# Optimization experiments

Hardware: AMD Instinct MI355X
Metric: run time of the kernel (lower is better)

The kernel has to match this reference:

```python
import jax, jax.numpy as jnp
import numpy as np
from itertools import combinations, permutations

B = 32768          # batch
LATENT = 9
H = 512            # hidden width
NB_OBJ = 5


def _make_o_ids():
    # 30 predicates: 10 unordered 'close' pairs then 20 ordered 'above' pairs.
    pairs = list(combinations(range(NB_OBJ), 2))
    perms = list(permutations(range(NB_OBJ), 2))
    ids = []
    for k in range(NB_OBJ):
        row = [i for i, p in enumerate(pairs) if k in p]
        row += [10 + i for i, p in enumerate(perms) if k in p]
        ids.append(row)
    return np.asarray(ids, dtype=np.int32)  # [5, 12]

O_IDS = jnp.asarray(_make_o_ids())


def setup_inputs() -> dict:
    key = jax.random.key(0)
    ks = jax.random.split(key, 20)
    w = lambda k, *s: (jax.random.normal(k, s, dtype=jnp.float32) * 0.05)
    return {
        "initial_c": jax.random.uniform(ks[0], (B, 30), dtype=jnp.float32),
        "initial_s": jax.random.normal(ks[1], (B, 15), dtype=jnp.float32),
        "current_c": jax.random.uniform(ks[2], (B, 30), dtype=jnp.float32),
        "eps": jax.random.normal(ks[3], (NB_OBJ, B, LATENT), dtype=jnp.float32),
        # encoder: 44 -> 512 -> 512, heads 512 -> 9
        "enc_W0": w(ks[4], H, 44), "enc_b0": w(ks[5], H),
        "enc_W1": w(ks[6], H, H), "enc_b1": w(ks[7], H),
        "Wm": w(ks[8], LATENT, H), "bm": w(ks[9], LATENT),
        "Wv": w(ks[10], LATENT, H), "bv": w(ks[11], LATENT),
        # decoder: 41 -> 512 -> 512 -> 12 (sigmoid)
        "dec_W0": w(ks[12], H, 41), "dec_b0": w(ks[13], H),
        "dec_W1": w(ks[14], H, H), "dec_b1": w(ks[15], H),
        "dec_W2": w(ks[16], 12, H), "dec_b2": w(ks[17], 12),
    }


def reference(initial_c, initial_s, current_c, eps,
              enc_W0, enc_b0, enc_W1, enc_b1, Wm, bm, Wv, bv,
              dec_W0, dec_b0, dec_W1, dec_b1, dec_W2, dec_b2):
    b = initial_c.shape[0]
    one_hot = jnp.broadcast_to(jnp.eye(NB_OBJ, dtype=initial_c.dtype)[:, None, :],
                               (NB_OBJ, b, NB_OBJ))              # [5,B,5]
    s_rep = jnp.broadcast_to(initial_s[None], (NB_OBJ, b, 15))    # [5,B,15]
    gi = jnp.transpose(initial_c[:, O_IDS], (1, 0, 2))            # [5,B,12]
    gc = jnp.transpose(current_c[:, O_IDS], (1, 0, 2))            # [5,B,12]

    # ---- encoder (ReLU after every layer, incl. last inner) ----
    x = jnp.concatenate([one_hot, s_rep, gi, gc], axis=-1)        # [5,B,44]
    h = jax.nn.relu(jnp.einsum('obi,hi->obh', x, enc_W0) + enc_b0)
    h = jax.nn.relu(jnp.einsum('obi,hi->obh', h, enc_W1) + enc_b1)
    means = jnp.einsum('obi,li->obl', h, Wm) + bm                 # [5,B,9]
    log_var = jnp.einsum('obi,li->obl', h, Wv) + bv               # [5,B,9]

    std = jnp.exp(0.5 * log_var)
    z = eps * std + means                                         # [5,B,9]

    # ---- decoder: ReLU x2, sigmoid head ----
    d = jnp.concatenate([one_hot, z, s_rep, gi], axis=-1)         # [5,B,41]
    h = jax.nn.relu(jnp.einsum('obi,hi->obh', d, dec_W0) + dec_b0)
    h = jax.nn.relu(jnp.einsum('obi,hi->obh', h, dec_W1) + dec_b1)
    recon_x = jax.nn.sigmoid(jnp.einsum('obi,li->obl', h, dec_W2) + dec_b2)  # [5,B,12]

    # scatter-add back into dense [B,30]
    reconstructed = jnp.zeros((b, 30), dtype=recon_x.dtype)
    reconstructed = reconstructed.at[:, O_IDS].add(jnp.transpose(recon_x, (1, 0, 2)))
    return (reconstructed, means, log_var, z)
```

## Files before the change

### kernel.cpp

```cpp
#include <hip/hip_runtime.h>
#include <math.h>

#define BATCH 32768
#define HID   512
#define NOBJ  5
#define TM    64
#define NBT   (BATCH/TM)

typedef __attribute__((ext_vector_type(8))) short bf16x8;
typedef __attribute__((ext_vector_type(4))) float f32x4;

typedef const __attribute__((address_space(1))) void* gas1_t;
typedef __attribute__((address_space(3))) void* las3_t;

__device__ __constant__ int d_OIDS[5][12] = {
  {0,1,2,3, 10,11,12,13,14,18,22,26},
  {0,4,5,6, 10,14,15,16,17,19,23,27},
  {1,4,7,8, 11,15,18,19,20,21,24,28},
  {2,5,7,9, 12,16,20,22,23,24,25,29},
  {3,6,8,9, 13,17,21,25,26,27,28,29}
};

#define UO_EW0   0
#define UO_EW1   (UO_EW0 + 512*64)
#define UO_HEADS (UO_EW1 + 512*512)
#define UO_DW0   (UO_HEADS + 32*512)
#define UO_DW1   (UO_DW0 + 512*64)
#define UO_DW2   (UO_DW1 + 512*512)
#define UO_TOTAL (UO_DW2 + 16*512)

#define OUT_MEANS (BATCH*30)
#define OUT_LV    (OUT_MEANS + NOBJ*BATCH*9)
#define OUT_Z     (OUT_LV    + NOBJ*BATCH*9)

__device__ __forceinline__ unsigned short f2b(float x) {
  unsigned int u = __builtin_bit_cast(unsigned int, x);
  u += 0x7FFFu + ((u >> 16) & 1u);
  return (unsigned short)(u >> 16);
}

__global__ void __launch_bounds__(256)
prep_bf16(const float* __restrict__ eW0, const float* __restrict__ eW1,
          const float* __restrict__ Wm,  const float* __restrict__ Wv,
          const float* __restrict__ dW0, const float* __restrict__ dW1,
          const float* __restrict__ dW2, unsigned short* __restrict__ ws)
{
  for (int i = blockIdx.x*blockDim.x + threadIdx.x; i < UO_TOTAL; i += gridDim.x*blockDim.x) {
    float v = 0.f; int j;
    if (i < UO_EW1) {
      j = i - UO_EW0; int h = j >> 6, k = j & 63;
      if (k < 44) v = eW0[h*44 + k];
    } else if (i < UO_HEADS) {
      j = i - UO_EW1; v = eW1[j];
    } else if (i < UO_DW0) {
      j = i - UO_HEADS; int r = j >> 9, k = j & 511;
      if (r < 9)                  v = Wm[r*512 + k];
      else if (r >= 16 && r < 25) v = Wv[(r-16)*512 + k];
    } else if (i < UO_DW1) {
      j = i - UO_DW0; int h = j >> 6, k = j & 63;
      if (k < 41) v = dW0[h*41 + k];
    } else if (i < UO_DW2) {
      j = i - UO_DW1; v = dW1[j];
    } else {
      j = i - UO_DW2; int r = j >> 9, k = j & 511;
      if (r < 12) v = dW2[r*512 + k];
    }
    ws[i] = f2b(v);
  }
}

template<int KDIM>
__device__ __forceinline__ void stage_B(const unsigned short* __restrict__ Wb, int kt,
                                        unsigned short* buf, int t)
{
  #pragma unroll
  for (int i = 0; i < 4; ++i) {
    const int c   = i*512 + t;
    const int col = c >> 2, j = c & 3;
    const int jp  = j ^ (col & 3);
    const unsigned short* g = Wb + col*KDIM + kt*32 + jp*8;
    unsigned short* l = buf + (i*512 + (t & ~63)) * 8;
    __builtin_amdgcn_global_load_lds((gas1_t)g, (las3_t)l, 16, 0, 0);
  }
}

template<int KT, int ROWW>
__device__ __forceinline__ void layer_mfma(const unsigned short* sIn,
                                           const unsigned short* __restrict__ Wb,
                                           const float* __restrict__ bias,
                                           unsigned short* sOut,
                                           unsigned short* sB,
                                           int wave, int lane, int t)
{
  const int lcol = lane & 15;
  const int kg   = lane >> 4;
  const int lk   = kg * 8;
  const int colbase = wave * 64;

  f32x4 acc[4][4];
  #pragma unroll
  for (int n = 0; n < 4; ++n) {
    const float bv = bias[colbase + n*16 + lcol];
    #pragma unroll
    for (int m = 0; m < 4; ++m) acc[m][n] = (f32x4){bv, bv, bv, bv};
  }

  stage_B<KT*32>(Wb, 0, sB, t);
  __syncthreads();

  int cur = 0;
  #pragma unroll 1
  for (int kt = 0; kt < KT; ++kt) {
    if (kt + 1 < KT) stage_B<KT*32>(Wb, kt + 1, sB + (cur ^ 1)*512*32, t);
    const unsigned short* bb = sB + cur*512*32;
    const int k0 = kt*32 + lk;
    bf16x8 a[4];
    #pragma unroll
    for (int m = 0; m < 4; ++m) {
      const int row = m*16 + lcol;
      a[m] = *(const bf16x8*)&sIn[row*ROWW + (k0 ^ ((row & 7) << 3))];
    }
    #pragma unroll
    for (int n = 0; n < 4; ++n) {
      const int col = colbase + n*16 + lcol;
      const bf16x8 b = *(const bf16x8*)&bb[col*32 + ((kg ^ (col & 3)) * 8)];
      #pragma unroll
      for (int m = 0; m < 4; ++m)
        acc[m][n] = __builtin_amdgcn_mfma_f32_16x16x32_bf16(a[m], b, acc[m][n], 0, 0, 0);
    }
    __syncthreads();
    cur ^= 1;
  }

  const int rbase = kg * 4;
  #pragma unroll
  for (int m = 0; m < 4; ++m)
    #pragma unroll
    for (int n = 0; n < 4; ++n) {
      const int col = colbase + n*16 + lcol;
      #pragma unroll
      for (int r = 0; r < 4; ++r) {
        const int row = m*16 + rbase + r;
        sOut[row*512 + (col ^ ((row & 7) << 3))] = f2b(fmaxf(acc[m][n][r], 0.f));
      }
    }
  __syncthreads();
}

__global__ void __launch_bounds__(512, 2)
vae_mfma(const float* __restrict__ initial_c, const float* __restrict__ initial_s,
         const float* __restrict__ current_c, const float* __restrict__ eps,
         const float* __restrict__ enc_b0, const float* __restrict__ enc_b1,
         const float* __restrict__ bm, const float* __restrict__ bv,
         const float* __restrict__ dec_b0, const float* __restrict__ dec_b1,
         const float* __restrict__ dec_b2, const unsigned short* __restrict__ ws,
         float* __restrict__ out)
{
  __shared__ __align__(16) unsigned short s_act[TM*512];
  __shared__ __align__(16) unsigned short s_bs[2*512*32];
  __shared__ __align__(16) unsigned short s_in[TM*64];

  const int t = threadIdx.x;
  const int wave = t >> 6, lane = t & 63;
  const int lcol = lane & 15, kg = lane >> 4;
  const int lk = kg * 8, rbase = kg * 4;
  const int o     = blockIdx.x / NBT;
  const int bbase = (blockIdx.x % NBT) * TM;

  for (int s = t; s < TM*64; s += 512) {
    const int row = s >> 6, col = s & 63;
    float v = 0.f;
    if (col < 5)       v = (col == o) ? 1.f : 0.f;
    else if (col < 20) v = initial_s[(bbase+row)*15 + col - 5];
    else if (col < 32) v = initial_c[(bbase+row)*30 + d_OIDS[o][col-20]];
    else if (col < 44) v = current_c[(bbase+row)*30 + d_OIDS[o][col-32]];
    s_in[row*64 + (col ^ ((row & 7) << 3))] = f2b(v);
  }
  __syncthreads();

  layer_mfma<2, 64>  (s_in,  ws + UO_EW0, enc_b0, s_act, s_bs, wave, lane, t);
  layer_mfma<16, 512>(s_act, ws + UO_EW1, enc_b1, s_act, s_bs, wave, lane, t);

  {
    for (int s = t; s < TM*64; s += 512) {
      const int row = s >> 6, col = s & 63;
      if (col >= 5 && col < 14) continue;
      float v = 0.f;
      if (col < 5)       v = (col == o) ? 1.f : 0.f;
      else if (col < 29) v = initial_s[(bbase+row)*15 + col - 14];
      else if (col < 41) v = initial_c[(bbase+row)*30 + d_OIDS[o][col-29]];
      s_in[row*64 + (col ^ ((row & 7) << 3))] = f2b(v);
    }
    f32x4 am, av;
    if (wave < 4) {
      const float bmv = (lcol < 9) ? bm[lcol] : 0.f;
      const float bvv = (lcol < 9) ? bv[lcol] : 0.f;
      am = (f32x4){bmv, bmv, bmv, bmv};
      av = (f32x4){bvv, bvv, bvv, bvv};
      const unsigned short* hpM = ws + UO_HEADS + lcol*512 + lk;
      const unsigned short* hpV = hpM + 16*512;
      const int hrow = wave*16 + lcol;
      bf16x8 m0 = *(const bf16x8*)hpM;
      bf16x8 v0 = *(const bf16x8*)hpV;
      #pragma unroll 1
      for (int kt = 0; kt < 16; ++kt) {
        bf16x8 m1 = m0, v1 = v0;
        if (kt + 1 < 16) {
          m1 = *(const bf16x8*)(hpM + (kt+1)*32);
          v1 = *(const bf16x8*)(hpV + (kt+1)*32);
        }
        const int k0 = kt*32 + lk;
        bf16x8 a = *(const bf16x8*)&s_act[hrow*512 + (k0 ^ ((lcol & 7) << 3))];
        am = __builtin_amdgcn_mfma_f32_16x16x32_bf16(a, m0, am, 0, 0, 0);
        av = __builtin_amdgcn_mfma_f32_16x16x32_bf16(a, v0, av, 0, 0, 0);
        m0 = m1; v0 = v1;
      }
    }
    __syncthreads();
    float* stage = (float*)s_bs;
    if (wave < 4 && lcol < 9) {
      #pragma unroll
      for (int r = 0; r < 4; ++r) {
        const int row = wave*16 + rbase + r;
        const int gid = (o*BATCH + bbase + row)*9 + lcol;
        const float m_ = am[r], v_ = av[r];
        const float zz = fmaf(eps[gid], expf(0.5f*v_), m_);
        stage[       row*9 + lcol] = m_;
        stage[576 +  row*9 + lcol] = v_;
        stage[1152 + row*9 + lcol] = zz;
        s_in[row*64 + ((5 + lcol) ^ ((row & 7) << 3))] = f2b(zz);
      }
    }
    __syncthreads();
    const int ob_m = OUT_MEANS + (o*BATCH + bbase)*9;
    const int ob_v = OUT_LV    + (o*BATCH + bbase)*9;
    const int ob_z = OUT_Z     + (o*BATCH + bbase)*9;
    for (int i = t; i < TM*9; i += 512) {
      __builtin_nontemporal_store(stage[i],        &out[ob_m + i]);
      __builtin_nontemporal_store(stage[576 + i],  &out[ob_v + i]);
      __builtin_nontemporal_store(stage[1152 + i], &out[ob_z + i]);
    }
    __syncthreads();
  }

  layer_mfma<2, 64>  (s_in,  ws + UO_DW0, dec_b0, s_act, s_bs, wave, lane, t);
  layer_mfma<16, 512>(s_act, ws + UO_DW1, dec_b1, s_act, s_bs, wave, lane, t);

  if (wave < 4) {
    const float b2 = (lcol < 12) ? dec_b2[lcol] : 0.f;
    f32x4 acc = (f32x4){b2, b2, b2, b2};
    const unsigned short* wp = ws + UO_DW2 + lcol*512 + lk;
    const int hrow = wave*16 + lcol;
    bf16x8 b0 = *(const bf16x8*)wp;
    #pragma unroll 1
    for (int kt = 0; kt < 16; ++kt) {
      bf16x8 b1 = b0;
      if (kt + 1 < 16) b1 = *(const bf16x8*)(wp + (kt+1)*32);
      const int k0 = kt*32 + lk;
      bf16x8 a = *(const bf16x8*)&s_act[hrow*512 + (k0 ^ ((lcol & 7) << 3))];
      acc = __builtin_amdgcn_mfma_f32_16x16x32_bf16(a, b0, acc, 0, 0, 0);
      b0 = b1;
    }
    if (lcol < 12) {
      const int c30 = d_OIDS[o][lcol];
      #pragma unroll
      for (int r = 0; r < 4; ++r) {
        const int row = wave*16 + rbase + r;
        atomicAdd(&out[(bbase + row)*30 + c30], 1.f / (1.f + expf(-acc[r])));
      }
    }
  }
}

__global__ void __launch_bounds__(256)
vae_naive(const float* __restrict__ initial_c, const float* __restrict__ initial_s,
          const float* __restrict__ current_c, const float* __restrict__ eps,
          const float* eW0, const float* eb0, const float* eW1, const float* eb1,
          const float* Wm, const float* bm, const float* Wv, const float* bv,
          const float* dW0, const float* db0, const float* dW1, const float* db1,
          const float* dW2, const float* db2, float* out)
{
  __shared__ float xs[44], ds[41], h1[HID], h2[HID], rec[30];
  const int b = blockIdx.x, t = threadIdx.x;
  if (t < 30) rec[t] = 0.f;
  for (int o = 0; o < NOBJ; ++o) {
    __syncthreads();
    if (t < 44) {
      float v;
      if      (t < 5)  v = (t == o) ? 1.f : 0.f;
      else if (t < 20) v = initial_s[b*15 + (t-5)];
      else if (t < 32) v = initial_c[b*30 + d_OIDS[o][t-20]];
      else             v = current_c[b*30 + d_OIDS[o][t-32]];
      xs[t] = v;
    }
    __syncthreads();
    for (int h = t; h < HID; h += 256) {
      float a = eb0[h];
      for (int k = 0; k < 44; ++k) a = fmaf(xs[k], eW0[h*44+k], a);
      h1[h] = fmaxf(a, 0.f);
    }
    __syncthreads();
    for (int h = t; h < HID; h += 256) {
      float a = eb1[h];
      for (int k = 0; k < HID; ++k) a = fmaf(h1[k], eW1[h*512+k], a);
      h2[h] = fmaxf(a, 0.f);
    }
    __syncthreads();
    if (t < 9) {
      float am = bm[t], av = bv[t];
      for (int k = 0; k < HID; ++k) { am = fmaf(h2[k], Wm[t*512+k], am); av = fmaf(h2[k], Wv[t*512+k], av); }
      const int gid = (o*BATCH + b)*9 + t;
      out[OUT_MEANS + gid] = am;
      out[OUT_LV    + gid] = av;
      const float zz = fmaf(eps[gid], expf(0.5f*av), am);
      out[OUT_Z     + gid] = zz;
      ds[5+t] = zz;
    }
    if (t < 41 && (t < 5 || t >= 14)) {
      float v;
      if      (t < 5)  v = (t == o) ? 1.f : 0.f;
      else if (t < 29) v = initial_s[b*15 + (t-14)];
      else             v = initial_c[b*30 + d_OIDS[o][t-29]];
      ds[t] = v;
    }
    __syncthreads();
    for (int h = t; h < HID; h += 256) {
      float a = db0[h];
      for (int k = 0; k < 41; ++k) a = fmaf(ds[k], dW0[h*41+k], a);
      h1[h] = fmaxf(a, 0.f);
    }
    __syncthreads();
    for (int h = t; h < HID; h += 256) {
      float a = db1[h];
      for (int k = 0; k < HID; ++k) a = fmaf(h1[k], dW1[h*512+k], a);
      h2[h] = fmaxf(a, 0.f);
    }
    __syncthreads();
    if (t < 12) {
      float a = db2[t];
      for (int k = 0; k < HID; ++k) a = fmaf(h2[k], dW2[t*512+k], a);
      rec[d_OIDS[o][t]] += 1.f / (1.f + expf(-a));
    }
  }
  __syncthreads();
  if (t < 30) out[b*30+t] = rec[t];
}

extern "C" void kernel_launch(void* const* d_in, const int* in_sizes, int n_in,
                              void* d_out, int out_size, void* d_ws, size_t ws_size,
                              hipStream_t stream)
{
  const float* initial_c = (const float*)d_in[0];
  const float* initial_s = (const float*)d_in[1];
  const float* current_c = (const float*)d_in[2];
  const float* eps       = (const float*)d_in[3];
  const float* eW0 = (const float*)d_in[4];
  const float* eb0 = (const float*)d_in[5];
  const float* eW1 = (const float*)d_in[6];
  const float* eb1 = (const float*)d_in[7];
  const float* Wm  = (const float*)d_in[8];
  const float* bm  = (const float*)d_in[9];
  const float* Wv  = (const float*)d_in[10];
  const float* bv  = (const float*)d_in[11];
  const float* dW0 = (const float*)d_in[12];
  const float* db0 = (const float*)d_in[13];
  const float* dW1 = (const float*)d_in[14];
  const float* db1 = (const float*)d_in[15];
  const float* dW2 = (const float*)d_in[16];
  const float* db2 = (const float*)d_in[17];
  float* out = (float*)d_out;

  if (ws_size >= (size_t)UO_TOTAL * sizeof(unsigned short)) {
    unsigned short* ws = (unsigned short*)d_ws;
    prep_bf16<<<1024, 256, 0, stream>>>(eW0, eW1, Wm, Wv, dW0, dW1, dW2, ws);
    hipMemsetAsync(out, 0, (size_t)BATCH * 30 * sizeof(float), stream);
    vae_mfma<<<NOBJ*NBT, 512, 0, stream>>>(initial_c, initial_s, current_c, eps,
                                           eb0, eb1, bm, bv, db0, db1, db2, ws, out);
  } else {
    vae_naive<<<BATCH, 256, 0, stream>>>(initial_c, initial_s, current_c, eps,
                                         eW0, eb0, eW1, eb1, Wm, bm, Wv, bv,
                                         dW0, db0, dW1, db1, dW2, db2, out);
  }
}
```

Measured before the change: 447.3 us.

## Triple-buffer weight staging with one barrier per k-step and fragment-ordered LDS layout

Weight tiles now go through a three-slot LDS ring and are prefetched two k-steps ahead. Each step waits on vmcnt with a single barrier instead of two __syncthreads. The staged B layout is rearranged so each lane's fragment is a contiguous 16-byte chunk, which removes the XOR swizzle on reads. MFMA sections run at raised wave priority. s_in is aliased into the third buffer slot to keep LDS usage unchanged, which risks corruption if the input tile is still live while layer 0 stages into that slot. The hand-written vmcnt counts also depend on exactly four outstanding loads per stage.

```diff
diff --git a/kernel.cpp b/kernel.cpp
--- a/kernel.cpp
+++ b/kernel.cpp
@@ -76,10 +76,10 @@
   #pragma unroll
   for (int i = 0; i < 4; ++i) {
     const int c   = i*512 + t;
-    const int col = c >> 2, j = c & 3;
-    const int jp  = j ^ (col & 3);
-    const unsigned short* g = Wb + col*KDIM + kt*32 + jp*8;
-    unsigned short* l = buf + (i*512 + (t & ~63)) * 8;
+    const int col = ((c >> 6) << 4) | (c & 15);
+    const int kg  = (c >> 4) & 3;
+    const unsigned short* g = Wb + col*KDIM + kt*32 + kg*8;
+    unsigned short* l = buf + (size_t)(i*512 + (t & ~63)) * 8;
     __builtin_amdgcn_global_load_lds((gas1_t)g, (las3_t)l, 16, 0, 0);
   }
 }
@@ -96,6 +96,7 @@
   const int kg   = lane >> 4;
   const int lk   = kg * 8;
   const int colbase = wave * 64;
+  const int cb4  = colbase >> 4;
 
   f32x4 acc[4][4];
   #pragma unroll
@@ -105,14 +106,21 @@
     for (int m = 0; m < 4; ++m) acc[m][n] = (f32x4){bv, bv, bv, bv};
   }
 
+  asm volatile("s_waitcnt vmcnt(0)" ::: "memory");
   stage_B<KT*32>(Wb, 0, sB, t);
-  __syncthreads();
+  if (KT > 1) stage_B<KT*32>(Wb, 1, sB + 16384, t);
 
   int cur = 0;
   #pragma unroll 1
   for (int kt = 0; kt < KT; ++kt) {
-    if (kt + 1 < KT) stage_B<KT*32>(Wb, kt + 1, sB + (cur ^ 1)*512*32, t);
-    const unsigned short* bb = sB + cur*512*32;
+    if (kt + 1 < KT) asm volatile("s_waitcnt vmcnt(4)" ::: "memory");
+    else             asm volatile("s_waitcnt vmcnt(0)" ::: "memory");
+    __builtin_amdgcn_s_barrier();
+    __builtin_amdgcn_sched_barrier(0);
+    int s2 = cur + 2; if (s2 >= 3) s2 -= 3;
+    if (kt + 2 < KT) stage_B<KT*32>(Wb, kt + 2, sB + s2*16384, t);
+
+    const unsigned short* bb = sB + cur*16384;
     const int k0 = kt*32 + lk;
     bf16x8 a[4];
     #pragma unroll
@@ -120,18 +128,20 @@
       const int row = m*16 + lcol;
       a[m] = *(const bf16x8*)&sIn[row*ROWW + (k0 ^ ((row & 7) << 3))];
     }
+    __builtin_amdgcn_s_setprio(1);
     #pragma unroll
     for (int n = 0; n < 4; ++n) {
-      const int col = colbase + n*16 + lcol;
-      const bf16x8 b = *(const bf16x8*)&bb[col*32 + ((kg ^ (col & 3)) * 8)];
+      const int chunk = ((cb4 + n)*4 + kg)*16 + lcol;
+      const bf16x8 b = *(const bf16x8*)&bb[chunk*8];
       #pragma unroll
       for (int m = 0; m < 4; ++m)
         acc[m][n] = __builtin_amdgcn_mfma_f32_16x16x32_bf16(a[m], b, acc[m][n], 0, 0, 0);
     }
-    __syncthreads();
-    cur ^= 1;
-  }
-
+    __builtin_amdgcn_s_setprio(0);
+    cur = (cur + 1 == 3) ? 0 : cur + 1;
+  }
+
+  __syncthreads();
   const int rbase = kg * 4;
   #pragma unroll
   for (int m = 0; m < 4; ++m)
@@ -157,8 +167,8 @@
          float* __restrict__ out)
 {
   __shared__ __align__(16) unsigned short s_act[TM*512];
-  __shared__ __align__(16) unsigned short s_bs[2*512*32];
-  __shared__ __align__(16) unsigned short s_in[TM*64];
+  __shared__ __align__(16) unsigned short s_bs[3*16384];
+  unsigned short* s_in = s_bs + 2*16384;
 
   const int t = threadIdx.x;
   const int wave = t >> 6, lane = t & 63;
```

Result: slower. 637.8 us (+42.6%).

## Double the row tile to 128 with a 2x4 wave grid and single-buffered B staging

Applied to the files above, without the earlier changes.

Raises the per-block row tile from 64 to 128 and arranges the 8 waves as a 2x4 grid, each computing 64x128 outputs, so every staged weight tile is reused across twice as many rows. The weight staging becomes single-buffered with a simpler, non-swizzled chunk layout. The input tile now aliases the activation buffer, which frees LDS. The cost is one block per CU instead of two (larger accumulator register footprint), the loss of load/compute overlap from double buffering, and possible LDS bank conflicts on the B reads.

```diff
diff --git a/kernel.cpp b/kernel.cpp
--- a/kernel.cpp
+++ b/kernel.cpp
@@ -4,7 +4,7 @@
 #define BATCH 32768
 #define HID   512
 #define NOBJ  5
-#define TM    64
+#define TM    128
 #define NBT   (BATCH/TM)
 
 typedef __attribute__((ext_vector_type(8))) short bf16x8;
@@ -76,10 +76,10 @@
   #pragma unroll
   for (int i = 0; i < 4; ++i) {
     const int c   = i*512 + t;
-    const int col = c >> 2, j = c & 3;
-    const int jp  = j ^ (col & 3);
-    const unsigned short* g = Wb + col*KDIM + kt*32 + jp*8;
-    unsigned short* l = buf + (i*512 + (t & ~63)) * 8;
+    const int col = ((c >> 6) << 4) | (c & 15);
+    const int kg  = (c >> 4) & 3;
+    const unsigned short* g = Wb + col*KDIM + kt*32 + kg*8;
+    unsigned short* l = buf + (size_t)(i*512 + (t & ~63)) * 8;
     __builtin_amdgcn_global_load_lds((gas1_t)g, (las3_t)l, 16, 0, 0);
   }
 }
@@ -90,64 +90,59 @@
                                            const float* __restrict__ bias,
                                            unsigned short* sOut,
                                            unsigned short* sB,
-                                           int wave, int lane, int t)
+                                           int wm, int wn, int lane, int t)
 {
   const int lcol = lane & 15;
   const int kg   = lane >> 4;
   const int lk   = kg * 8;
-  const int colbase = wave * 64;
-
-  f32x4 acc[4][4];
+  const int colbase = wn * 128;
+  const int rowbase = wm * 64;
+  const int swz = (lcol & 7) << 3;
+
+  f32x4 acc[4][8];
   #pragma unroll
-  for (int n = 0; n < 4; ++n) {
+  for (int n = 0; n < 8; ++n) {
     const float bv = bias[colbase + n*16 + lcol];
     #pragma unroll
     for (int m = 0; m < 4; ++m) acc[m][n] = (f32x4){bv, bv, bv, bv};
   }
 
-  stage_B<KT*32>(Wb, 0, sB, t);
-  __syncthreads();
-
-  int cur = 0;
   #pragma unroll 1
   for (int kt = 0; kt < KT; ++kt) {
-    if (kt + 1 < KT) stage_B<KT*32>(Wb, kt + 1, sB + (cur ^ 1)*512*32, t);
-    const unsigned short* bb = sB + cur*512*32;
+    stage_B<KT*32>(Wb, kt, sB, t);
     const int k0 = kt*32 + lk;
     bf16x8 a[4];
     #pragma unroll
-    for (int m = 0; m < 4; ++m) {
-      const int row = m*16 + lcol;
-      a[m] = *(const bf16x8*)&sIn[row*ROWW + (k0 ^ ((row & 7) << 3))];
-    }
+    for (int m = 0; m < 4; ++m)
+      a[m] = *(const bf16x8*)&sIn[(rowbase + m*16 + lcol)*ROWW + (k0 ^ swz)];
+    __syncthreads();
     #pragma unroll
-    for (int n = 0; n < 4; ++n) {
-      const int col = colbase + n*16 + lcol;
-      const bf16x8 b = *(const bf16x8*)&bb[col*32 + ((kg ^ (col & 3)) * 8)];
+    for (int n = 0; n < 8; ++n) {
+      const int chunk = ((wn*8 + n)*4 + kg)*16 + lcol;
+      const bf16x8 b = *(const bf16x8*)&sB[chunk*8];
       #pragma unroll
       for (int m = 0; m < 4; ++m)
         acc[m][n] = __builtin_amdgcn_mfma_f32_16x16x32_bf16(a[m], b, acc[m][n], 0, 0, 0);
     }
     __syncthreads();
-    cur ^= 1;
   }
 
   const int rbase = kg * 4;
   #pragma unroll
   for (int m = 0; m < 4; ++m)
     #pragma unroll
-    for (int n = 0; n < 4; ++n) {
+    for (int n = 0; n < 8; ++n) {
       const int col = colbase + n*16 + lcol;
       #pragma unroll
       for (int r = 0; r < 4; ++r) {
-        const int row = m*16 + rbase + r;
+        const int row = rowbase + m*16 + rbase + r;
         sOut[row*512 + (col ^ ((row & 7) << 3))] = f2b(fmaxf(acc[m][n][r], 0.f));
       }
     }
   __syncthreads();
 }
 
-__global__ void __launch_bounds__(512, 2)
+__global__ void __launch_bounds__(512, 1)
 vae_mfma(const float* __restrict__ initial_c, const float* __restrict__ initial_s,
          const float* __restrict__ current_c, const float* __restrict__ eps,
          const float* __restrict__ enc_b0, const float* __restrict__ enc_b1,
@@ -157,11 +152,12 @@
          float* __restrict__ out)
 {
   __shared__ __align__(16) unsigned short s_act[TM*512];
-  __shared__ __align__(16) unsigned short s_bs[2*512*32];
-  __shared__ __align__(16) unsigned short s_in[TM*64];
+  __shared__ __align__(16) unsigned short s_bs[16384];
+  unsigned short* s_in = s_act;
 
   const int t = threadIdx.x;
   const int wave = t >> 6, lane = t & 63;
+  const int wm = wave >> 2, wn = wave & 3;
   const int lcol = lane & 15, kg = lane >> 4;
   const int lk = kg * 8, rbase = kg * 4;
   const int o     = blockIdx.x / NBT;
@@ -178,21 +174,12 @@
   }
   __syncthreads();
 
-  layer_mfma<2, 64>  (s_in,  ws + UO_EW0, enc_b0, s_act, s_bs, wave, lane, t);
-  layer_mfma<16, 512>(s_act, ws + UO_EW1, enc_b1, s_act, s_bs, wave, lane, t);
+  layer_mfma<2, 64>  (s_in,  ws + UO_EW0, enc_b0, s_act, s_bs, wm, wn, lane, t);
+  layer_mfma<16, 512>(s_act, ws + UO_EW1, enc_b1, s_act, s_bs, wm, wn, lane, t);
 
   {
-    for (int s = t; s < TM*64; s += 512) {
-      const int row = s >> 6, col = s & 63;
-      if (col >= 5 && col < 14) continue;
-      float v = 0.f;
-      if (col < 5)       v = (col == o) ? 1.f : 0.f;
-      else if (col < 29) v = initial_s[(bbase+row)*15 + col - 14];
-      else if (col < 41) v = initial_c[(bbase+row)*30 + d_OIDS[o][col-29]];
-      s_in[row*64 + (col ^ ((row & 7) << 3))] = f2b(v);
-    }
     f32x4 am, av;
-    if (wave < 4) {
+    {
       const float bmv = (lcol < 9) ? bm[lcol] : 0.f;
       const float bvv = (lcol < 9) ? bv[lcol] : 0.f;
       am = (f32x4){bmv, bmv, bmv, bmv};
@@ -217,17 +204,27 @@
       }
     }
     __syncthreads();
-    float* stage = (float*)s_bs;
-    if (wave < 4 && lcol < 9) {
+
+    for (int s = t; s < TM*64; s += 512) {
+      const int row = s >> 6, col = s & 63;
+      if (col >= 5 && col < 14) continue;
+      float v = 0.f;
+      if (col < 5)       v = (col == o) ? 1.f : 0.f;
+      else if (col < 29) v = initial_s[(bbase+row)*15 + col - 14];
+      else if (col < 41) v = initial_c[(bbase+row)*30 + d_OIDS[o][col-29]];
+      s_in[row*64 + (col ^ ((row & 7) << 3))] = f2b(v);
+    }
+    float* stage = (float*)(s_act + 8192);
+    if (lcol < 9) {
       #pragma unroll
       for (int r = 0; r < 4; ++r) {
         const int row = wave*16 + rbase + r;
         const int gid = (o*BATCH + bbase + row)*9 + lcol;
         const float m_ = am[r], v_ = av[r];
         const float zz = fmaf(eps[gid], expf(0.5f*v_), m_);
-        stage[       row*9 + lcol] = m_;
-        stage[576 +  row*9 + lcol] = v_;
-        stage[1152 + row*9 + lcol] = zz;
+        stage[        row*9 + lcol] = m_;
+        stage[1152 +  row*9 + lcol] = v_;
+        stage[2304 +  row*9 + lcol] = zz;
         s_in[row*64 + ((5 + lcol) ^ ((row & 7) << 3))] = f2b(zz);
       }
     }
@@ -237,16 +234,15 @@
     const int ob_z = OUT_Z     + (o*BATCH + bbase)*9;
     for (int i = t; i < TM*9; i += 512) {
       __builtin_nontemporal_store(stage[i],        &out[ob_m + i]);
-      __builtin_nontemporal_store(stage[576 + i],  &out[ob_v + i]);
-      __builtin_nontemporal_store(stage[1152 + i], &out[ob_z + i]);
-    }
-    __syncthreads();
-  }
-
-  layer_mfma<2, 64>  (s_in,  ws + UO_DW0, dec_b0, s_act, s_bs, wave, lane, t);
-  layer_mfma<16, 512>(s_act, ws + UO_DW1, dec_b1, s_act, s_bs, wave, lane, t);
-
-  if (wave < 4) {
+      __builtin_nontemporal_store(stage[1152 + i], &out[ob_v + i]);
+      __builtin_nontemporal_store(stage[2304 + i], &out[ob_z + i]);
+    }
+  }
+
+  layer_mfma<2, 64>  (s_in,  ws + UO_DW0, dec_b0, s_act, s_bs, wm, wn, lane, t);
+  layer_mfma<16, 512>(s_act, ws + UO_DW1, dec_b1, s_act, s_bs, wm, wn, lane, t);
+
+  {
     const float b2 = (lcol < 12) ? dec_b2[lcol] : 0.f;
     f32x4 acc = (f32x4){b2, b2, b2, b2};
     const unsigned short* wp = ws + UO_DW2 + lcol*512 + lk;
@@ -265,7 +261,7 @@
       const int c30 = d_OIDS[o][lcol];
       #pragma unroll
       for (int r = 0; r < 4; ++r) {
-        const int row = wave*16 + rbase + r;
+        const int row = hrow - lcol + rbase + r;
         atomicAdd(&out[(bbase + row)*30 + c30], 1.f / (1.f + expf(-acc[r])));
       }
     }
```

Result: slower. 567.2 us (+26.8%).

## Load weight fragments directly to registers instead of LDS staging

Applied to the files above, without the earlier changes.

Replaces the LDS double-buffered staging of weight tiles (global_load_lds plus a barrier per k-step) with per-wave direct global loads of B fragments into a two-deep register pipeline, unrolled by two k-steps. This removes the per-iteration block barriers and frees the 64KB weight staging buffer, which may allow two blocks per CU. The cost is higher register pressure and exposure to global/L2 latency on the weight loads, which are now hidden only by register prefetch.

```diff
diff --git a/kernel.cpp b/kernel.cpp
--- a/kernel.cpp
+++ b/kernel.cpp
@@ -9,9 +9,6 @@
 
 typedef __attribute__((ext_vector_type(8))) short bf16x8;
 typedef __attribute__((ext_vector_type(4))) float f32x4;
-
-typedef const __attribute__((address_space(1))) void* gas1_t;
-typedef __attribute__((address_space(3))) void* las3_t;
 
 __device__ __constant__ int d_OIDS[5][12] = {
   {0,1,2,3, 10,11,12,13,14,18,22,26},
@@ -69,33 +66,18 @@
   }
 }
 
-template<int KDIM>
-__device__ __forceinline__ void stage_B(const unsigned short* __restrict__ Wb, int kt,
-                                        unsigned short* buf, int t)
-{
-  #pragma unroll
-  for (int i = 0; i < 4; ++i) {
-    const int c   = i*512 + t;
-    const int col = c >> 2, j = c & 3;
-    const int jp  = j ^ (col & 3);
-    const unsigned short* g = Wb + col*KDIM + kt*32 + jp*8;
-    unsigned short* l = buf + (i*512 + (t & ~63)) * 8;
-    __builtin_amdgcn_global_load_lds((gas1_t)g, (las3_t)l, 16, 0, 0);
-  }
-}
-
 template<int KT, int ROWW>
 __device__ __forceinline__ void layer_mfma(const unsigned short* sIn,
                                            const unsigned short* __restrict__ Wb,
                                            const float* __restrict__ bias,
                                            unsigned short* sOut,
-                                           unsigned short* sB,
-                                           int wave, int lane, int t)
+                                           int wave, int lane)
 {
   const int lcol = lane & 15;
   const int kg   = lane >> 4;
   const int lk   = kg * 8;
   const int colbase = wave * 64;
+  const int swz = (lcol & 7) << 3;
 
   f32x4 acc[4][4];
   #pragma unroll
@@ -105,33 +87,53 @@
     for (int m = 0; m < 4; ++m) acc[m][n] = (f32x4){bv, bv, bv, bv};
   }
 
-  stage_B<KT*32>(Wb, 0, sB, t);
+  const unsigned short* wpn[4];
+  #pragma unroll
+  for (int n = 0; n < 4; ++n)
+    wpn[n] = Wb + (size_t)(colbase + n*16 + lcol)*(KT*32) + lk;
+
+  bf16x8 a0[4], a1[4], b0[4], b1[4];
+  #pragma unroll
+  for (int n = 0; n < 4; ++n) b0[n] = *(const bf16x8*)(wpn[n]);
+  #pragma unroll
+  for (int n = 0; n < 4; ++n) b1[n] = *(const bf16x8*)(wpn[n] + 32);
+  #pragma unroll
+  for (int m = 0; m < 4; ++m)
+    a0[m] = *(const bf16x8*)&sIn[(m*16 + lcol)*ROWW + (lk ^ swz)];
+
+  #pragma unroll 1
+  for (int kt = 0; kt < KT; kt += 2) {
+    {
+      const int k1 = (kt+1)*32 + lk;
+      #pragma unroll
+      for (int m = 0; m < 4; ++m)
+        a1[m] = *(const bf16x8*)&sIn[(m*16 + lcol)*ROWW + (k1 ^ swz)];
+    }
+    #pragma unroll
+    for (int n = 0; n < 4; ++n)
+      #pragma unroll
+      for (int m = 0; m < 4; ++m)
+        acc[m][n] = __builtin_amdgcn_mfma_f32_16x16x32_bf16(a0[m], b0[n], acc[m][n], 0, 0, 0);
+    if (kt + 2 < KT) {
+      #pragma unroll
+      for (int n = 0; n < 4; ++n) b0[n] = *(const bf16x8*)(wpn[n] + (kt+2)*32);
+      const int k2 = (kt+2)*32 + lk;
+      #pragma unroll
+      for (int m = 0; m < 4; ++m)
+        a0[m] = *(const bf16x8*)&sIn[(m*16 + lcol)*ROWW + (k2 ^ swz)];
+    }
+    #pragma unroll
+    for (int n = 0; n < 4; ++n)
+      #pragma unroll
+      for (int m = 0; m < 4; ++m)
+        acc[m][n] = __builtin_amdgcn_mfma_f32_16x16x32_bf16(a1[m], b1[n], acc[m][n], 0, 0, 0);
+    if (kt + 3 < KT) {
+      #pragma unroll
+      for (int n = 0; n < 4; ++n) b1[n] = *(const bf16x8*)(wpn[n] + (kt+3)*32);
+    }
+  }
+
   __syncthreads();
-
-  int cur = 0;
-  #pragma unroll 1
-  for (int kt = 0; kt < KT; ++kt) {
-    if (kt + 1 < KT) stage_B<KT*32>(Wb, kt + 1, sB + (cur ^ 1)*512*32, t);
-    const unsigned short* bb = sB + cur*512*32;
-    const int k0 = kt*32 + lk;
-    bf16x8 a[4];
-    #pragma unroll
-    for (int m = 0; m < 4; ++m) {
-      const int row = m*16 + lcol;
-      a[m] = *(const bf16x8*)&sIn[row*ROWW + (k0 ^ ((row & 7) << 3))];
-    }
-    #pragma unroll
-    for (int n = 0; n < 4; ++n) {
-      const int col = colbase + n*16 + lcol;
-      const bf16x8 b = *(const bf16x8*)&bb[col*32 + ((kg ^ (col & 3)) * 8)];
-      #pragma unroll
-      for (int m = 0; m < 4; ++m)
-        acc[m][n] = __builtin_amdgcn_mfma_f32_16x16x32_bf16(a[m], b, acc[m][n], 0, 0, 0);
-    }
-    __syncthreads();
-    cur ^= 1;
-  }
-
   const int rbase = kg * 4;
   #pragma unroll
   for (int m = 0; m < 4; ++m)
@@ -157,8 +159,8 @@
          float* __restrict__ out)
 {
   __shared__ __align__(16) unsigned short s_act[TM*512];
-  __shared__ __align__(16) unsigned short s_bs[2*512*32];
   __shared__ __align__(16) unsigned short s_in[TM*64];
+  __shared__ float s_stage[3*TM*9];
 
   const int t = threadIdx.x;
   const int wave = t >> 6, lane = t & 63;
@@ -178,8 +180,8 @@
   }
   __syncthreads();
 
-  layer_mfma<2, 64>  (s_in,  ws + UO_EW0, enc_b0, s_act, s_bs, wave, lane, t);
-  layer_mfma<16, 512>(s_act, ws + UO_EW1, enc_b1, s_act, s_bs, wave, lane, t);
+  layer_mfma<2, 64>  (s_in,  ws + UO_EW0, enc_b0, s_act, wave, lane);
+  layer_mfma<16, 512>(s_act, ws + UO_EW1, enc_b1, s_act, wave, lane);
 
   {
     for (int s = t; s < TM*64; s += 512) {
@@ -217,7 +219,6 @@
       }
     }
     __syncthreads();
-    float* stage = (float*)s_bs;
     if (wave < 4 && lcol < 9) {
       #pragma unroll
       for (int r = 0; r < 4; ++r) {
@@ -225,9 +226,9 @@
         const int gid = (o*BATCH + bbase + row)*9 + lcol;
         const float m_ = am[r], v_ = av[r];
         const float zz = fmaf(eps[gid], expf(0.5f*v_), m_);
-        stage[       row*9 + lcol] = m_;
-        stage[576 +  row*9 + lcol] = v_;
-        stage[1152 + row*9 + lcol] = zz;
+        s_stage[        row*9 + lcol] = m_;
+        s_stage[576 +   row*9 + lcol] = v_;
+        s_stage[1152 +  row*9 + lcol] = zz;
         s_in[row*64 + ((5 + lcol) ^ ((row & 7) << 3))] = f2b(zz);
       }
     }
@@ -236,15 +237,14 @@
     const int ob_v = OUT_LV    + (o*BATCH + bbase)*9;
     const int ob_z = OUT_Z     + (o*BATCH + bbase)*9;
     for (int i = t; i < TM*9; i += 512) {
-      __builtin_nontemporal_store(stage[i],        &out[ob_m + i]);
-      __builtin_nontemporal_store(stage[576 + i],  &out[ob_v + i]);
-      __builtin_nontemporal_store(stage[1152 + i], &out[ob_z + i]);
-    }
-    __syncthreads();
-  }
-
-  layer_mfma<2, 64>  (s_in,  ws + UO_DW0, dec_b0, s_act, s_bs, wave, lane, t);
-  layer_mfma<16, 512>(s_act, ws + UO_DW1, dec_b1, s_act, s_bs, wave, lane, t);
+      __builtin_nontemporal_store(s_stage[i],        &out[ob_m + i]);
+      __builtin_nontemporal_store(s_stage[576 + i],  &out[ob_v + i]);
+      __builtin_nontemporal_store(s_stage[1152 + i], &out[ob_z + i]);
+    }
+  }
+
+  layer_mfma<2, 64>  (s_in,  ws + UO_DW0, dec_b0, s_act, wave, lane);
+  layer_mfma<16, 512>(s_act, ws + UO_DW1, dec_b1, s_act, wave, lane);
 
   if (wave < 4) {
     const float b2 = (lcol < 12) ? dec_b2[lcol] : 0.f;
```

New measurement: 513.1 us. 1.15x slower.
